# Performance work log

Hardware: AMD Instinct MI355X
Metric: run time of the kernel (lower is better)

Reference implementation:

```python
import jax, jax.numpy as jnp
import numpy as np

B, D, H, W, C = 2, 8, 128, 128, 64
HEADS, DH = 4, 16
EPS = 1e-12  # torch F.normalize eps


def setup_inputs() -> dict:
    key = jax.random.key(0)
    ks = jax.random.split(key, 8)
    rn = lambda k, shp, s: jax.random.normal(k, shp, jnp.float32) * s
    return {
        "x_in": rn(ks[0], (B, D, H, W, C), 1.0),
        "Wq": rn(ks[1], (C, HEADS * DH), 0.05),
        "Wk": rn(ks[2], (C, HEADS * DH), 0.05),
        "Wv": rn(ks[3], (C, HEADS * DH), 0.05),
        "rescale": jnp.ones((HEADS, 1, 1), jnp.float32),
        "Wproj": rn(ks[4], (HEADS * DH, C), 0.05),
        "bproj": jnp.zeros((C,), jnp.float32),
        "Wpos1": rn(ks[5], (C, 1, 3, 3, 3), 0.1),
        "Wpos2": rn(ks[6], (C, 1, 3, 3, 3), 0.1),
    }


def _l2norm(x):
    # torch F.normalize(p=2, dim=-1): x / max(||x||, eps)
    return x / jnp.maximum(jnp.linalg.norm(x, axis=-1, keepdims=True), EPS)


def _dwconv3d(x, w):
    # depthwise Conv3d, kernel 3, stride 1, padding 1, groups = channels
    return jax.lax.conv_general_dilated(
        x, w, (1, 1, 1), 'SAME',
        dimension_numbers=('NCDHW', 'OIDHW', 'NCDHW'),
        feature_group_count=w.shape[0])


def reference(x_in, Wq, Wk, Wv, rescale, Wproj, bproj, Wpos1, Wpos2):
    b, d, h, w, c = x_in.shape
    n = d * h * w
    x = x_in.reshape(b, n, c)
    v_inp = x @ Wv                                   # [b, n, heads*dh]
    # [b, heads, dh, n] layout (attention over channel dim)
    q = jnp.transpose((x @ Wq).reshape(b, n, HEADS, DH), (0, 2, 3, 1))
    k = jnp.transpose((x @ Wk).reshape(b, n, HEADS, DH), (0, 2, 3, 1))
    v = jnp.transpose(v_inp.reshape(b, n, HEADS, DH), (0, 2, 3, 1))
    q = _l2norm(q)
    k = _l2norm(k)
    attn = jnp.einsum('bhdn,bhen->bhde', k, q) * rescale  # [b, heads, dh, dh]
    attn = jax.nn.softmax(attn, axis=-1)
    out = jnp.einsum('bhde,bhen->bhdn', attn, v)          # [b, heads, dh, n]
    out = jnp.transpose(out, (0, 3, 1, 2)).reshape(b, n, HEADS * DH)
    out_c = (out @ Wproj + bproj).reshape(b, d, h, w, c)
    # positional branch: depthwise conv -> GELU -> depthwise conv on v_inp
    vv = jnp.transpose(v_inp.reshape(b, d, h, w, c), (0, 4, 1, 2, 3))  # NCDHW
    p = _dwconv3d(vv, Wpos1)
    p = jax.nn.gelu(p, approximate=False)
    p = _dwconv3d(p, Wpos2)
    out_p = jnp.transpose(p, (0, 2, 3, 4, 1))
    return out_c + out_p
```

## Files before the change

kernel.cpp:

```cpp
#include <hip/hip_runtime.h>
#include <math.h>

#define DD 8
#define HH 128
#define WW2 128
#define NPT 131072
#define NTOT 262144
#define NBK 16

typedef __attribute__((ext_vector_type(8))) short short8;
typedef __attribute__((ext_vector_type(4))) float f32x4;
typedef __attribute__((ext_vector_type(4))) unsigned short u16x4;
typedef __attribute__((ext_vector_type(8))) unsigned short u16x8;
typedef unsigned short u16;

static const size_t OFF_P1  = 0;
static const size_t OFF_P2  = 33554432;
static const size_t OFF_V   = 67108864;
static const size_t OFF_PW  = 100663296;
static const size_t OFF_PM  = 100687872;
static const size_t OFF_FLAG= 100704256;
static const size_t OFF_CW  = 100704768;
static const size_t OFF_PART= 134217728;
#define SP_F    0
#define WQ_F    131072
#define WK_F    135168
#define CW_WPROJ 0
#define CW_WPOS1 4096
#define CW_WPOS2 5824
#define CW_RESC  7552
#define CW_BPROJ 7556

__device__ __forceinline__ float bf2f(u16 u){
  unsigned int x = ((unsigned int)u) << 16;
  return __builtin_bit_cast(float, x);
}
__device__ __forceinline__ u16 f2bf(float f){
  unsigned int x = __builtin_bit_cast(unsigned int, f);
  unsigned int r = (x + 0x7fffu + ((x >> 16) & 1u)) >> 16;
  return (u16)r;
}

__device__ __forceinline__ float fgelu(float o){
  float z  = o * 0.70710678118654752f;
  float az = fabsf(z);
  float t1 = __builtin_amdgcn_rcpf(fmaf(0.3275911f, az, 1.f));
  float poly = t1 * fmaf(t1, fmaf(t1, fmaf(t1, fmaf(t1, 1.061405429f,
               -1.453152027f), 1.421413741f), -0.284496736f), 0.254829592f);
  float ex = __expf(-z * z);
  float er = 1.f - poly * ex;
  er = (z < 0.f) ? -er : er;
  return 0.5f * o * (1.f + er);
}

__device__ __forceinline__ int probe_isf32(const void* x, int t){
  u16 u = ((const u16*)x)[2 * (t & 63)];
  int e = (u >> 7) & 0xFF;
  int plaus = (u == 0) || (u == 0x8000u) || (e >= 100 && e <= 130);
  unsigned long long m = __ballot(plaus);
  return (__popcll(m) < 48) ? 1 : 0;
}

__global__ __launch_bounds__(256) void k_prep(const void* __restrict__ x,
    const void* __restrict__ Wproj, const void* __restrict__ rescale,
    const void* __restrict__ bproj, const void* __restrict__ Wpos1,
    const void* __restrict__ Wpos2, const void* __restrict__ Wq,
    const void* __restrict__ Wk, const void* __restrict__ Wv,
    int* __restrict__ flag, float* __restrict__ cw, float* __restrict__ gpart,
    u16* __restrict__ packW){
  __shared__ int sflag;
  int t = threadIdx.x, blk = blockIdx.x;
  if (t < 64){
    int f = probe_isf32(x, t);
    if (t == 0) sflag = f;
  }
  __syncthreads();
  int isf32 = sflag;
  if (blk < 32){
    for (int i = blk * 4096 + t; i < (blk + 1) * 4096; i += 256)
      gpart[i] = 0.f;
    if (blk == 0){
      if (t == 0) *flag = isf32;
      auto conv = [&](const void* src, float* dst, int n){
        for (int i = t; i < n; i += 256)
          dst[i] = isf32 ? ((const float*)src)[i] : bf2f(((const u16*)src)[i]);
      };
      conv(Wproj, cw + CW_WPROJ, 4096);
      conv(Wpos1, cw + CW_WPOS1, 1728);
      conv(Wpos2, cw + CW_WPOS2, 1728);
      conv(rescale, cw + CW_RESC, 4);
      conv(bproj,   cw + CW_BPROJ, 64);
      conv(Wq, gpart + WQ_F, 4096);
      conv(Wk, gpart + WK_F, 4096);
    }
  } else {
    int o = (blk - 32) * 256 + t;
    int f = o >> 9, l = (o >> 3) & 63, j = o & 7;
    int tt = f >> 1, s = f & 1;
    int k = s * 32 + (l >> 4) * 8 + j;
    int n = tt * 16 + (l & 15);
    int idx = k * 64 + n;
    float val = isf32 ? ((const float*)Wv)[idx] : bf2f(((const u16*)Wv)[idx]);
    packW[o] = f2bf(val);
  }
}

__device__ __forceinline__ short8 ld8_adapt(const void* p, size_t idx, int isf32){
  if (!isf32) return *(const short8*)((const u16*)p + idx);
  const float4* f = (const float4*)((const float*)p + idx);
  float4 u = f[0], v2 = f[1];
  short8 r;
  r[0] = (short)f2bf(u.x);  r[1] = (short)f2bf(u.y);
  r[2] = (short)f2bf(u.z);  r[3] = (short)f2bf(u.w);
  r[4] = (short)f2bf(v2.x); r[5] = (short)f2bf(v2.y);
  r[6] = (short)f2bf(v2.z); r[7] = (short)f2bf(v2.w);
  return r;
}

__global__ __launch_bounds__(512) void k_qkv(const void* __restrict__ x,
                                             const int* __restrict__ flag,
                                             const u16* __restrict__ packW,
                                             u16* __restrict__ vT,
                                             float* __restrict__ Sp){
  __shared__ u16 sXT[64][136];
  int isf32 = *flag;
  int wave = threadIdx.x >> 6, lane = threadIdx.x & 63;
  int m = lane & 15, quad = lane >> 4;
  const short8* bw = (const short8*)packW;
  short8 bv[8];
#pragma unroll
  for (int f = 0; f < 8; f++) bv[f] = bw[f * 64 + lane];
  int c1 = wave >> 1, c2p = (wave & 1) * 2;
  f32x4 aS[2];
  aS[0] = (f32x4)(0.f); aS[1] = (f32x4)(0.f);

  int pbase = blockIdx.x * 1024;
  int b = pbase >> 17;

  for (int s = 0; s < 8; s++){
    int p0 = pbase + s * 128 + wave * 16;
    size_t rowbase = (size_t)(p0 + m) * 64;
    short8 a0 = ld8_adapt(x, rowbase + quad * 8, isf32);
    short8 a1 = ld8_adapt(x, rowbase + 32 + quad * 8, isf32);
    f32x4 av[4];
#pragma unroll
    for (int t = 0; t < 4; t++) av[t] = (f32x4)(0.f);
#pragma unroll
    for (int t = 0; t < 4; t++){
      av[t] = __builtin_amdgcn_mfma_f32_16x16x32_bf16(a0, bv[t * 2 + 0], av[t], 0, 0, 0);
      av[t] = __builtin_amdgcn_mfma_f32_16x16x32_bf16(a1, bv[t * 2 + 1], av[t], 0, 0, 0);
    }
    int nloc = p0 & (NPT - 1);
#pragma unroll
    for (int t = 0; t < 4; t++){
      u16x4 pk;
#pragma unroll
      for (int r = 0; r < 4; r++) pk[r] = f2bf(av[t][r]);
      *(u16x4*)(vT + ((size_t)(b * 64 + t * 16 + m)) * NPT + nloc + quad * 4) = pk;
    }
    if (s) __syncthreads();
#pragma unroll
    for (int j = 0; j < 8; j++){
      sXT[quad * 8 + j][wave * 16 + m]      = (u16)a0[j];
      sXT[32 + quad * 8 + j][wave * 16 + m] = (u16)a1[j];
    }
    __syncthreads();
#pragma unroll
    for (int ks = 0; ks < 4; ks++){
      short8 fA  = *(const short8*)&sXT[c1 * 16 + m][ks * 32 + quad * 8];
      short8 fB0 = *(const short8*)&sXT[(c2p + 0) * 16 + m][ks * 32 + quad * 8];
      short8 fB1 = *(const short8*)&sXT[(c2p + 1) * 16 + m][ks * 32 + quad * 8];
      aS[0] = __builtin_amdgcn_mfma_f32_16x16x32_bf16(fA, fB0, aS[0], 0, 0, 0);
      aS[1] = __builtin_amdgcn_mfma_f32_16x16x32_bf16(fA, fB1, aS[1], 0, 0, 0);
    }
  }
  int bk = blockIdx.x & (NBK - 1);
  float* Sb = Sp + (size_t)(bk * 2 + b) * 4096;
#pragma unroll
  for (int tt = 0; tt < 2; tt++)
#pragma unroll
    for (int r = 0; r < 4; r++)
      atomicAdd(&Sb[(c1 * 16 + quad * 4 + r) * 64 + (c2p + tt) * 16 + m], aS[tt][r]);
}

__global__ __launch_bounds__(256) void k_attn_h(const float* __restrict__ Sp,
    const float* __restrict__ wqk, const float* __restrict__ cw,
    u16* __restrict__ packM){
  __shared__ float sS[64 * 65];
  __shared__ float sWh[1024];
  __shared__ float sT[1024];
  __shared__ float sG[256];
  __shared__ float sA[256];
  __shared__ float sNq[16], sNk[16];
  int blk = blockIdx.x, t = threadIdx.x;
  int b = blk >> 2, h = blk & 3;
  for (int i = t; i < 4096; i += 256){
    float s = 0.f;
#pragma unroll
    for (int bk = 0; bk < NBK; bk++) s += Sp[(size_t)(bk * 2 + b) * 4096 + i];
    sS[(i >> 6) * 65 + (i & 63)] = s;
  }
  for (int i = t; i < 1024; i += 256)
    sWh[i] = wqk[(i >> 4) * 64 + h * 16 + (i & 15)];
  __syncthreads();
  int cc = t & 63, eg = t >> 6;
  {
    float a0 = 0.f, a1 = 0.f, a2 = 0.f, a3 = 0.f;
    for (int c2 = 0; c2 < 64; c2++){
      float sv = sS[cc * 65 + c2];
      a0 = fmaf(sv, sWh[c2 * 16 + eg * 4 + 0], a0);
      a1 = fmaf(sv, sWh[c2 * 16 + eg * 4 + 1], a1);
      a2 = fmaf(sv, sWh[c2 * 16 + eg * 4 + 2], a2);
      a3 = fmaf(sv, sWh[c2 * 16 + eg * 4 + 3], a3);
    }
    sT[cc * 16 + eg * 4 + 0] = a0;
    sT[cc * 16 + eg * 4 + 1] = a1;
    sT[cc * 16 + eg * 4 + 2] = a2;
    sT[cc * 16 + eg * 4 + 3] = a3;
  }
  __syncthreads();
  if (t < 16){
    float a = 0.f;
    for (int c = 0; c < 64; c++) a += sWh[c * 16 + t] * sT[c * 16 + t];
    sNq[t] = a;
  }
  __syncthreads();
  for (int i = t; i < 1024; i += 256)
    sWh[i] = wqk[4096 + (i >> 4) * 64 + h * 16 + (i & 15)];
  __syncthreads();
  {
    int d = t >> 4, e = t & 15;
    float a = 0.f;
    for (int c = 0; c < 64; c++) a += sWh[c * 16 + d] * sT[c * 16 + e];
    sG[d * 16 + e] = a;
  }
  __syncthreads();
  {
    float a0 = 0.f, a1 = 0.f, a2 = 0.f, a3 = 0.f;
    for (int c2 = 0; c2 < 64; c2++){
      float sv = sS[cc * 65 + c2];
      a0 = fmaf(sv, sWh[c2 * 16 + eg * 4 + 0], a0);
      a1 = fmaf(sv, sWh[c2 * 16 + eg * 4 + 1], a1);
      a2 = fmaf(sv, sWh[c2 * 16 + eg * 4 + 2], a2);
      a3 = fmaf(sv, sWh[c2 * 16 + eg * 4 + 3], a3);
    }
    __syncthreads();
    sT[cc * 16 + eg * 4 + 0] = a0;
    sT[cc * 16 + eg * 4 + 1] = a1;
    sT[cc * 16 + eg * 4 + 2] = a2;
    sT[cc * 16 + eg * 4 + 3] = a3;
  }
  __syncthreads();
  if (t < 16){
    float a = 0.f;
    for (int c = 0; c < 64; c++) a += sWh[c * 16 + t] * sT[c * 16 + t];
    sNk[t] = a;
  }
  __syncthreads();
  for (int i = t; i < 1024; i += 256)
    sT[i] = cw[CW_WPROJ + (h * 16 + (i >> 6)) * 64 + (i & 63)];
  if (t < 16){
    int d = t;
    float nk = fmaxf(sqrtf(sNk[d]), 1e-12f);
    float rs = cw[CW_RESC + h];
    float lg[16]; float mx = -1e30f;
#pragma unroll
    for (int e = 0; e < 16; e++){
      float nq = fmaxf(sqrtf(sNq[e]), 1e-12f);
      float L = sG[d * 16 + e] / (nk * nq) * rs;
      lg[e] = L; mx = fmaxf(mx, L);
    }
    float sum = 0.f;
#pragma unroll
    for (int e = 0; e < 16; e++){ lg[e] = expf(lg[e] - mx); sum += lg[e]; }
    float inv = 1.f / sum;
#pragma unroll
    for (int e = 0; e < 16; e++) sA[d * 16 + e] = lg[e] * inv;
  }
  __syncthreads();
#pragma unroll
  for (int q = 0; q < 4; q++){
    int i = q * 256 + t;
    int t4 = i >> 8, lhi = (i >> 7) & 1, llo = (i >> 3) & 15, j = i & 7;
    int e = lhi * 8 + j, c = t4 * 16 + llo;
    float acc = 0.f;
#pragma unroll
    for (int d = 0; d < 16; d++) acc += sA[d * 16 + e] * sT[d * 64 + c];
    int f = t4 * 2 + (h >> 1);
    int l = (2 * (h & 1) + lhi) * 16 + llo;
    packM[b * 4096 + f * 512 + l * 8 + j] = f2bf(acc);
  }
}

template <bool GELU>
__global__ __launch_bounds__(256, 4) void k_dwconv(const u16* __restrict__ src,
    const float* __restrict__ wpos, u16* __restrict__ dst){
  int xi = threadIdx.x & 15, ty = threadIdx.x >> 4;
  int zp = ty >> 2, yq = ty & 3;
  int x0 = xi * 8;
  int c  = blockIdx.x;
  int y0 = blockIdx.y * 8 + yq * 2;
  int b  = blockIdx.z;
  int z0 = zp * 2;
  const float* wg = wpos + c * 27;
  float w27[27];
#pragma unroll
  for (int i = 0; i < 27; i++) w27[i] = wg[i];
  const u16* plane = src + (size_t)(b * 64 + c) * NPT;

  short8 raw[16];
  const short8 zz8 = (short8)0;
#pragma unroll
  for (int iz = 0; iz < 4; iz++){
    int zz = z0 - 1 + iz;
    int zc = zz < 0 ? 0 : (zz > DD - 1 ? DD - 1 : zz);
    int zv = (zz == zc);
#pragma unroll
    for (int iy = 0; iy < 4; iy++){
      int yy = y0 - 1 + iy;
      int yc = yy < 0 ? 0 : (yy > HH - 1 ? HH - 1 : yy);
      short8 v = *(const short8*)(plane + zc * 16384 + yc * 128 + x0);
      raw[iz * 4 + iy] = (zv && yy == yc) ? v : zz8;
    }
  }

  float acc[2][2][8];
#pragma unroll
  for (int dz = 0; dz < 2; dz++)
#pragma unroll
    for (int dy = 0; dy < 2; dy++)
#pragma unroll
      for (int xx = 0; xx < 8; xx++) acc[dz][dy][xx] = 0.f;

#pragma unroll
  for (int iz = 0; iz < 4; iz++){
#pragma unroll
    for (int iy = 0; iy < 4; iy++){
      short8 mid = raw[iz * 4 + iy];
      float row[10];
#pragma unroll
      for (int e = 0; e < 8; e++) row[1 + e] = bf2f((u16)mid[e]);
      float lf = __shfl_up(row[8], 1);
      float rg = __shfl_down(row[1], 1);
      row[0] = (xi > 0)  ? lf : 0.f;
      row[9] = (xi < 15) ? rg : 0.f;
#pragma unroll
      for (int dzi = 0; dzi < 2; dzi++){
        int kd = iz - dzi;
        if (kd < 0 || kd > 2) continue;
#pragma unroll
        for (int dyi = 0; dyi < 2; dyi++){
          int kh = iy - dyi;
          if (kh < 0 || kh > 2) continue;
#pragma unroll
          for (int kw = 0; kw < 3; kw++){
            float w = w27[kd * 9 + kh * 3 + kw];
#pragma unroll
            for (int xx = 0; xx < 8; xx++)
              acc[dzi][dyi][xx] = fmaf(row[xx + kw], w, acc[dzi][dyi][xx]);
          }
        }
      }
    }
  }
#pragma unroll
  for (int dzi = 0; dzi < 2; dzi++){
    int zo = z0 + dzi;
#pragma unroll
    for (int dyi = 0; dyi < 2; dyi++){
      int yo = y0 + dyi;
      u16x8 pk;
#pragma unroll
      for (int xx = 0; xx < 8; xx++){
        float o = acc[dzi][dyi][xx];
        if (GELU) o = fgelu(o);
        pk[xx] = f2bf(o);
      }
      *(u16x8*)(dst + (size_t)(b * 64 + c) * NPT + zo * 16384 + yo * 128 + x0) = pk;
    }
  }
}

__global__ __launch_bounds__(256) void k_final(const u16* __restrict__ vT,
                                               const u16* __restrict__ packM,
                                               const float* __restrict__ bprojf,
                                               const u16* __restrict__ p2T,
                                               float* __restrict__ out){
  __shared__ u16 sP2[64][72];
  __shared__ u16 sVt[64][72];
  __shared__ float sOut[64][68];
  int tid = threadIdx.x;
  int wave = tid >> 6, lane = tid & 63;
  int m = lane & 15, quad = lane >> 4;
  int pbase = blockIdx.x * 64;
  int b = pbase >> 17;
  int nloc = pbase & (NPT - 1);
  {
    int c = tid >> 2, po = (tid & 3) * 16;
    const u16* s1 = p2T + (size_t)(b * 64 + c) * NPT + nloc + po;
    *(u16x8*)&sP2[c][po]     = *(const u16x8*)s1;
    *(u16x8*)&sP2[c][po + 8] = *(const u16x8*)(s1 + 8);
    const u16* s2 = vT + (size_t)(b * 64 + c) * NPT + nloc + po;
    *(u16x8*)&sVt[c][po]     = *(const u16x8*)s2;
    *(u16x8*)&sVt[c][po + 8] = *(const u16x8*)(s2 + 8);
  }
  __syncthreads();
  int lp = wave * 16 + m;
  short8 a0, a1;
#pragma unroll
  for (int j = 0; j < 8; j++){
    a0[j] = (short)sVt[quad * 8 + j][lp];
    a1[j] = (short)sVt[32 + quad * 8 + j][lp];
  }
  const short8* bm = (const short8*)(packM + (size_t)b * 4096);
  f32x4 acc[4];
#pragma unroll
  for (int t = 0; t < 4; t++) acc[t] = (f32x4)(0.f);
#pragma unroll
  for (int t = 0; t < 4; t++){
    short8 b0 = bm[(t * 2 + 0) * 64 + lane];
    short8 b1 = bm[(t * 2 + 1) * 64 + lane];
    acc[t] = __builtin_amdgcn_mfma_f32_16x16x32_bf16(a0, b0, acc[t], 0, 0, 0);
    acc[t] = __builtin_amdgcn_mfma_f32_16x16x32_bf16(a1, b1, acc[t], 0, 0, 0);
  }
#pragma unroll
  for (int t = 0; t < 4; t++){
    int c = t * 16 + m;
    float bias = bprojf[c];
#pragma unroll
    for (int r = 0; r < 4; r++){
      int op = wave * 16 + quad * 4 + r;
      sOut[op][c] = acc[t][r] + bias + bf2f(sP2[c][op]);
    }
  }
  __syncthreads();
  int hi = tid >> 4, lo = tid & 15;
#pragma unroll
  for (int k = 0; k < 4; k++){
    int pos = k * 16 + hi;
    int c0  = lo * 4;
    float4 v = *(const float4*)&sOut[pos][c0];
    *(float4*)(out + (size_t)(pbase + pos) * 64 + c0) = v;
  }
}

extern "C" void kernel_launch(void* const* d_in, const int* in_sizes, int n_in,
                              void* d_out, int out_size, void* d_ws, size_t ws_size,
                              hipStream_t stream){
  (void)in_sizes; (void)n_in; (void)out_size; (void)ws_size;
  const void* x      = d_in[0];
  const void* Wq     = d_in[1];
  const void* Wk     = d_in[2];
  const void* Wv     = d_in[3];
  const void* rescale= d_in[4];
  const void* Wproj  = d_in[5];
  const void* bproj  = d_in[6];
  const void* Wpos1  = d_in[7];
  const void* Wpos2  = d_in[8];

  char* ws = (char*)d_ws;
  u16* p1T   = (u16*)(ws + OFF_P1);
  u16* p2T   = (u16*)(ws + OFF_P2);
  u16* vT    = (u16*)(ws + OFF_V);
  u16* packW = (u16*)(ws + OFF_PW);
  u16* packM = (u16*)(ws + OFF_PM);
  int* flag  = (int*)(ws + OFF_FLAG);
  float* cw  = (float*)(ws + OFF_CW);
  float* part= (float*)(ws + OFF_PART);
  float* Sp  = part + SP_F;
  float* wqk = part + WQ_F;
  float* out = (float*)d_out;

  k_prep<<<48, 256, 0, stream>>>(x, Wproj, rescale, bproj, Wpos1, Wpos2, Wq, Wk, Wv,
                                 flag, cw, Sp, packW);
  k_qkv<<<NTOT / 1024, 512, 0, stream>>>(x, flag, packW, vT, Sp);
  k_attn_h<<<8, 256, 0, stream>>>(Sp, wqk, cw, packM);
  k_dwconv<true><<<dim3(64, 16, 2), 256, 0, stream>>>(vT, cw + CW_WPOS1, p1T);
  k_dwconv<false><<<dim3(64, 16, 2), 256, 0, stream>>>(p1T, cw + CW_WPOS2, p2T);
  k_final<<<NTOT / 64, 256, 0, stream>>>(vT, packM, cw + CW_BPROJ, p2T, out);
}
```

Before: 244.8 us.

## Fuse both depthwise 3D convs into one kernel with LDS halo tiles

Replaces the two separate depthwise conv launches with a single kernel. It loads a v tile with a 2-row y halo into shared memory, computes conv1 plus GELU into a shared intermediate with a 1-row halo, then runs conv2 from shared memory. This removes the write and re-read of the p1 intermediate in global memory and one launch. In exchange it recomputes the halo rows of conv1, uses more LDS per block, and runs at lower occupancy (launch bounds 3).

New measurement: 258.5 us. +5.6%, slower.

```diff
diff --git a/kernel.cpp b/kernel.cpp
--- a/kernel.cpp
+++ b/kernel.cpp
@@ -292,92 +292,122 @@
   }
 }
 
-template <bool GELU>
-__global__ __launch_bounds__(256, 4) void k_dwconv(const u16* __restrict__ src,
-    const float* __restrict__ wpos, u16* __restrict__ dst){
-  int xi = threadIdx.x & 15, ty = threadIdx.x >> 4;
-  int zp = ty >> 2, yq = ty & 3;
-  int x0 = xi * 8;
+__global__ __launch_bounds__(256, 3) void k_convf2(const u16* __restrict__ src,
+    const float* __restrict__ wpos1, const float* __restrict__ wpos2,
+    u16* __restrict__ dst){
+  __shared__ u16 sV[8][12][136];
+  __shared__ u16 sP[8][10][136];
+  int tid = threadIdx.x;
   int c  = blockIdx.x;
-  int y0 = blockIdx.y * 8 + yq * 2;
+  int y0 = blockIdx.y * 8;
   int b  = blockIdx.z;
-  int z0 = zp * 2;
-  const float* wg = wpos + c * 27;
-  float w27[27];
-#pragma unroll
-  for (int i = 0; i < 27; i++) w27[i] = wg[i];
   const u16* plane = src + (size_t)(b * 64 + c) * NPT;
 
-  short8 raw[16];
-  const short8 zz8 = (short8)0;
-#pragma unroll
-  for (int iz = 0; iz < 4; iz++){
-    int zz = z0 - 1 + iz;
-    int zc = zz < 0 ? 0 : (zz > DD - 1 ? DD - 1 : zz);
-    int zv = (zz == zc);
-#pragma unroll
-    for (int iy = 0; iy < 4; iy++){
-      int yy = y0 - 1 + iy;
-      int yc = yy < 0 ? 0 : (yy > HH - 1 ? HH - 1 : yy);
-      short8 v = *(const short8*)(plane + zc * 16384 + yc * 128 + x0);
-      raw[iz * 4 + iy] = (zv && yy == yc) ? v : zz8;
-    }
-  }
-
-  float acc[2][2][8];
-#pragma unroll
-  for (int dz = 0; dz < 2; dz++)
-#pragma unroll
-    for (int dy = 0; dy < 2; dy++)
-#pragma unroll
-      for (int xx = 0; xx < 8; xx++) acc[dz][dy][xx] = 0.f;
-
-#pragma unroll
-  for (int iz = 0; iz < 4; iz++){
-#pragma unroll
-    for (int iy = 0; iy < 4; iy++){
-      short8 mid = raw[iz * 4 + iy];
-      float row[10];
-#pragma unroll
-      for (int e = 0; e < 8; e++) row[1 + e] = bf2f((u16)mid[e]);
-      float lf = __shfl_up(row[8], 1);
-      float rg = __shfl_down(row[1], 1);
-      row[0] = (xi > 0)  ? lf : 0.f;
-      row[9] = (xi < 15) ? rg : 0.f;
-#pragma unroll
-      for (int dzi = 0; dzi < 2; dzi++){
-        int kd = iz - dzi;
-        if (kd < 0 || kd > 2) continue;
-#pragma unroll
-        for (int dyi = 0; dyi < 2; dyi++){
-          int kh = iy - dyi;
-          if (kh < 0 || kh > 2) continue;
-#pragma unroll
-          for (int kw = 0; kw < 3; kw++){
-            float w = w27[kd * 9 + kh * 3 + kw];
-#pragma unroll
-            for (int xx = 0; xx < 8; xx++)
-              acc[dzi][dyi][xx] = fmaf(row[xx + kw], w, acc[dzi][dyi][xx]);
-          }
+#pragma unroll
+  for (int k = 0; k < 6; k++){
+    int sid = k * 256 + tid;
+    int z  = sid / 192;
+    int rem = sid - z * 192;
+    int jy = rem >> 4, xi = rem & 15;
+    int ay = y0 - 2 + jy;
+    int ayc = ay < 0 ? 0 : (ay > HH - 1 ? HH - 1 : ay);
+    u16x8 v = *(const u16x8*)(plane + z * 16384 + ayc * 128 + xi * 8);
+    if (ay != ayc) v = (u16x8)(u16)0;
+    *(u16x8*)&sV[z][jy][1 + xi * 8] = v;
+    if (xi == 0)  sV[z][jy][0]   = 0;
+    if (xi == 15) sV[z][jy][129] = 0;
+  }
+  float w1[27];
+#pragma unroll
+  for (int i = 0; i < 27; i++) w1[i] = wpos1[c * 27 + i];
+  __syncthreads();
+
+#pragma unroll
+  for (int k = 0; k < 5; k++){
+    int sid = k * 256 + tid;
+    int z  = sid / 160;
+    int rem = sid - z * 160;
+    int j = rem >> 4, xi = rem & 15;
+    float acc[8];
+#pragma unroll
+    for (int e = 0; e < 8; e++) acc[e] = 0.f;
+#pragma unroll
+    for (int kd = 0; kd < 3; kd++){
+      int zz = z - 1 + kd;
+      int zc = zz < 0 ? 0 : (zz > 7 ? 7 : zz);
+      float zm = (zz == zc) ? 1.f : 0.f;
+#pragma unroll
+      for (int kh = 0; kh < 3; kh++){
+        const u16* rp = &sV[zc][j + kh][xi * 8];
+        u16x8 ra = *(const u16x8*)rp;
+        u16x4 r4 = *(const u16x4*)(rp + 8);
+        float rb[10];
+#pragma unroll
+        for (int e = 0; e < 8; e++) rb[e] = bf2f((u16)ra[e]);
+        rb[8] = bf2f((u16)r4[0]);
+        rb[9] = bf2f((u16)r4[1]);
+#pragma unroll
+        for (int kw = 0; kw < 3; kw++){
+          float w = w1[kd * 9 + kh * 3 + kw] * zm;
+#pragma unroll
+          for (int xx = 0; xx < 8; xx++)
+            acc[xx] = fmaf(rb[xx + kw], w, acc[xx]);
         }
       }
     }
-  }
-#pragma unroll
-  for (int dzi = 0; dzi < 2; dzi++){
-    int zo = z0 + dzi;
-#pragma unroll
-    for (int dyi = 0; dyi < 2; dyi++){
-      int yo = y0 + dyi;
-      u16x8 pk;
-#pragma unroll
-      for (int xx = 0; xx < 8; xx++){
-        float o = acc[dzi][dyi][xx];
-        if (GELU) o = fgelu(o);
-        pk[xx] = f2bf(o);
+    int ay = y0 - 1 + j;
+    int valid = (ay >= 0 && ay < HH);
+    u16x8 pk;
+#pragma unroll
+    for (int xx = 0; xx < 8; xx++)
+      pk[xx] = valid ? f2bf(fgelu(acc[xx])) : (u16)0;
+    *(u16x8*)&sP[z][j][1 + xi * 8] = pk;
+    if (xi == 0)  sP[z][j][0]   = 0;
+    if (xi == 15) sP[z][j][129] = 0;
+  }
+  float w2[27];
+#pragma unroll
+  for (int i = 0; i < 27; i++) w2[i] = wpos2[c * 27 + i];
+  __syncthreads();
+
+#pragma unroll
+  for (int k = 0; k < 4; k++){
+    int sid = k * 256 + tid;
+    int z  = sid >> 7;
+    int rem = sid & 127;
+    int r = rem >> 4, xi = rem & 15;
+    float acc[8];
+#pragma unroll
+    for (int e = 0; e < 8; e++) acc[e] = 0.f;
+#pragma unroll
+    for (int kd = 0; kd < 3; kd++){
+      int zz = z - 1 + kd;
+      int zc = zz < 0 ? 0 : (zz > 7 ? 7 : zz);
+      float zm = (zz == zc) ? 1.f : 0.f;
+#pragma unroll
+      for (int kh = 0; kh < 3; kh++){
+        const u16* rp = &sP[zc][r + kh][xi * 8];
+        u16x8 ra = *(const u16x8*)rp;
+        u16x4 r4 = *(const u16x4*)(rp + 8);
+        float rb[10];
+#pragma unroll
+        for (int e = 0; e < 8; e++) rb[e] = bf2f((u16)ra[e]);
+        rb[8] = bf2f((u16)r4[0]);
+        rb[9] = bf2f((u16)r4[1]);
+#pragma unroll
+        for (int kw = 0; kw < 3; kw++){
+          float w = w2[kd * 9 + kh * 3 + kw] * zm;
+#pragma unroll
+          for (int xx = 0; xx < 8; xx++)
+            acc[xx] = fmaf(rb[xx + kw], w, acc[xx]);
+        }
       }
-      *(u16x8*)(dst + (size_t)(b * 64 + c) * NPT + zo * 16384 + yo * 128 + x0) = pk;
-    }
+    }
+    u16x8 pk;
+#pragma unroll
+    for (int xx = 0; xx < 8; xx++) pk[xx] = f2bf(acc[xx]);
+    *(u16x8*)(dst + (size_t)(b * 64 + c) * NPT + z * 16384 +
+              (size_t)(y0 + r) * 128 + xi * 8) = pk;
   }
 }
 
@@ -459,7 +489,6 @@
   const void* Wpos2  = d_in[8];
 
   char* ws = (char*)d_ws;
-  u16* p1T   = (u16*)(ws + OFF_P1);
   u16* p2T   = (u16*)(ws + OFF_P2);
   u16* vT    = (u16*)(ws + OFF_V);
   u16* packW = (u16*)(ws + OFF_PW);
@@ -475,7 +504,6 @@
                                  flag, cw, Sp, packW);
   k_qkv<<<NTOT / 1024, 512, 0, stream>>>(x, flag, packW, vT, Sp);
   k_attn_h<<<8, 256, 0, stream>>>(Sp, wqk, cw, packM);
-  k_dwconv<true><<<dim3(64, 16, 2), 256, 0, stream>>>(vT, cw + CW_WPOS1, p1T);
-  k_dwconv<false><<<dim3(64, 16, 2), 256, 0, stream>>>(p1T, cw + CW_WPOS2, p2T);
+  k_convf2<<<dim3(64, 16, 2), 256, 0, stream>>>(vT, cw + CW_WPOS1, cw + CW_WPOS2, p2T);
   k_final<<<NTOT / 64, 256, 0, stream>>>(vT, packM, cw + CW_BPROJ, p2T, out);
 }
```
